# Optimization experiments

Hardware: AMD Instinct MI355X
Metric: run time of the kernel (lower is better)

## Reference

```python
import jax, jax.numpy as jnp
import numpy as np

WS = 4           # window_size
NUM_HEADS = 4
LN_EPS = 1e-5


def setup_inputs() -> dict:
    key = jax.random.key(0)
    ks = jax.random.split(key, 8)
    d = 256
    s = 0.02
    return {
        "feature": jax.random.normal(ks[0], (8, d, 127, 127), dtype=jnp.float32),
        "ln_w": jnp.ones((d,), jnp.float32),
        "ln_b": jnp.zeros((d,), jnp.float32),
        "in_w": jax.random.normal(ks[1], (3 * d, d), jnp.float32) * s,
        "in_b": jnp.zeros((3 * d,), jnp.float32),
        "out_w": jax.random.normal(ks[2], (d, d), jnp.float32) * s,
        "out_b": jnp.zeros((d,), jnp.float32),
        "proj_w": jax.random.normal(ks[3], (d, d), jnp.float32) * s,
        "proj_b": jnp.zeros((d,), jnp.float32),
    }


def reference(feature, ln_w, ln_b, in_w, in_b, out_w, out_b, proj_w, proj_b):
    B, C, H, W = feature.shape
    ws = WS
    pad_h = (-H) % ws
    pad_w = (-W) % ws
    x = jnp.pad(feature, ((0, 0), (0, 0), (0, pad_h), (0, pad_w)))
    Hp, Wp = H + pad_h, W + pad_w
    nh, nw = Hp // ws, Wp // ws
    # NCHW -> NHWC -> windows [B*nh*nw, ws*ws, C]
    x = x.transpose(0, 2, 3, 1)
    win = (x.reshape(B, nh, ws, nw, ws, C)
            .transpose(0, 1, 3, 2, 4, 5)
            .reshape(-1, ws * ws, C))
    # LayerNorm (ddof=0, matches torch)
    mu = win.mean(-1, keepdims=True)
    var = win.var(-1, keepdims=True)
    xn = (win - mu) / jnp.sqrt(var + LN_EPS) * ln_w + ln_b
    # fused QKV projection, then split heads
    qkv = xn @ in_w.T + in_b
    q, k, v = jnp.split(qkv, 3, axis=-1)
    hd = C // NUM_HEADS
    def heads(t):
        return t.reshape(t.shape[0], t.shape[1], NUM_HEADS, hd).transpose(0, 2, 1, 3)
    q, k, v = heads(q), heads(k), heads(v)
    scores = jnp.einsum('bhqd,bhkd->bhqk', q, k) / np.float32(np.sqrt(hd))
    a = jax.nn.softmax(scores, axis=-1)
    o = jnp.einsum('bhqk,bhkd->bhqd', a, v)
    o = o.transpose(0, 2, 1, 3).reshape(-1, ws * ws, C)
    o = o @ out_w.T + out_b
    # residual + Linear + exact GELU
    y = win + jax.nn.gelu(o @ proj_w.T + proj_b, approximate=False)
    # windows -> NHWC, crop padding, -> NCHW
    y = (y.reshape(B, nh, nw, ws, ws, C)
          .transpose(0, 1, 3, 2, 4, 5)
          .reshape(B, Hp, Wp, C))
    return y[:, :H, :W, :].transpose(0, 3, 1, 2)
```

## Files before the change

### kernel.cpp

```cpp
#include <hip/hip_runtime.h>

typedef _Float16 f16;
typedef __attribute__((ext_vector_type(4))) _Float16 half4;
typedef __attribute__((ext_vector_type(8))) _Float16 half8;
typedef __attribute__((ext_vector_type(4))) float f32x4;
typedef unsigned short u16;

#define MFMA32(a,b,c) __builtin_amdgcn_mfma_f32_16x16x32_f16(a,b,c,0,0,0)
#define MFMA16(a,b,c) __builtin_amdgcn_mfma_f32_16x16x16f16(a,b,c,0,0,0)

#define W_IN0   0
#define W_OUT0  196608
#define W_PROJ0 262144
#define X0      327680
#define QK0     33882112ull
#define VT0     100990976ull

__device__ __forceinline__ float gelu_f(float x) {
    float z = x * 0.70710678118f;
    float az = fabsf(z);
    float t = 1.f / (1.f + 0.3275911f * az);
    float e = __expf(-z * z);
    float poly = ((((1.061405429f * t - 1.453152027f) * t + 1.421413741f) * t
                   - 0.284496736f) * t + 0.254829592f) * t;
    float er = 1.f - poly * e;
    er = copysignf(er, z);
    return 0.5f * x * (1.f + er);
}

__global__ void k0_cast(const float* __restrict__ iw, const float* __restrict__ ow,
                        const float* __restrict__ pw, f16* __restrict__ W) {
    int i = blockIdx.x * 256 + threadIdx.x;
    if (i < 196608) W[W_IN0 + i] = (f16)iw[i];
    if (i < 16384) {
        const int s = i & 8191;
        const float* src = (i < 8192) ? ow : pw;
        f16* dst = W + ((i < 8192) ? W_OUT0 : W_PROJ0);
        const int g  = s & 3;
        const int r  = (s >> 2) & 31;
        const int kc = (s >> 7) & 7;
        const int ch = s >> 10;
        const int R = ch * 32 + r;
        const int c0 = kc * 32 + g * 4;
        f32x4 v0 = *(const f32x4*)(src + R * 256 + c0);
        f32x4 v1 = *(const f32x4*)(src + R * 256 + c0 + 16);
        half8 o;
#pragma unroll
        for (int j = 0; j < 4; ++j) { o[j] = (f16)v0[j]; o[j + 4] = (f16)v1[j]; }
        const int sg = g ^ ((r >> 1) & 3);
        *(half8*)(dst + ch * 8192 + kc * 1024 + r * 32 + sg * 8) = o;
    }
}

__global__ __launch_bounds__(256, 2)
void k1_pack(const float* __restrict__ feat, const float* __restrict__ lnw,
             const float* __restrict__ lnb, f16* __restrict__ X) {
    __shared__ float redS[256], redQ[256];
    const int tid = threadIdx.x;
    const int w = tid & 127, cq = tid >> 7;
    const int bid = blockIdx.x;
    const int bb = bid >> 7, h = bid & 127;
    const int c0 = cq * 128;
    const bool ok = (h < 127) && (w < 127);
    const size_t bbase = (size_t)bb * (256 * 127 * 127);
    const float* p0 = feat + bbase + (size_t)c0 * 16129 + (size_t)h * 127 + w;

    half8 ov[16];
    float s = 0.f, s2 = 0.f;
    if (ok) {
#pragma unroll
        for (int i = 0; i < 16; ++i) {
            half8 hv;
#pragma unroll
            for (int j = 0; j < 8; ++j) {
                float v = p0[(size_t)(i * 8 + j) * 16129];
                s += v; s2 += v * v; hv[j] = (f16)v;
            }
            ov[i] = hv;
        }
    } else {
#pragma unroll
        for (int i = 0; i < 16; ++i) {
            half8 hv;
#pragma unroll
            for (int j = 0; j < 8; ++j) hv[j] = (f16)0.f;
            ov[i] = hv;
        }
    }
    redS[tid] = s; redQ[tid] = s2;
    __syncthreads();
    float st = redS[w] + redS[w + 128];
    float qt = redQ[w] + redQ[w + 128];
    float mu = st * (1.f / 256.f);
    float rs = rsqrtf(qt * (1.f / 256.f) - mu * mu + 1e-5f);

    const int wi = h >> 2, hh = h & 3;
    const int jh = w >> 5, wl4 = (w >> 2) & 7, e = w & 3;
    const size_t t = ((size_t)((bb * 32 + wi) * 4 + jh)) * 128 + wl4 * 16 + hh * 4 + e;
    f16* xrow = X + t * 256 + c0;
#pragma unroll
    for (int i = 0; i < 16; ++i) {
        f32x4 lw0 = *(const f32x4*)(lnw + c0 + i * 8);
        f32x4 lw1 = *(const f32x4*)(lnw + c0 + i * 8 + 4);
        f32x4 lb0 = *(const f32x4*)(lnb + c0 + i * 8);
        f32x4 lb1 = *(const f32x4*)(lnb + c0 + i * 8 + 4);
        half8 o;
#pragma unroll
        for (int j = 0; j < 4; ++j) {
            o[j]     = (f16)(((float)ov[i][j]     - mu) * rs * lw0[j] + lb0[j]);
            o[j + 4] = (f16)(((float)ov[i][j + 4] - mu) * rs * lw1[j] + lb1[j]);
        }
        *(half8*)(xrow + i * 8) = o;
    }
}

__global__ __launch_bounds__(512, 2)
void k2_qkv(const f16* __restrict__ X, const f16* __restrict__ win,
            const float* __restrict__ inb, f16* __restrict__ QK, f16* __restrict__ VT) {
    __shared__ __align__(16) char sm[73728];
    const int tid = threadIdx.x, lane = tid & 63, wv = tid >> 6;
    const int nwg = gridDim.x;
    const int bid = (blockIdx.x & 7) * (nwg >> 3) + (blockIdx.x >> 3);
    const int mt = bid / 6, nb = bid % 6;
    const size_t Mbase = (size_t)mt * 256;
    const int n0 = nb * 128;
    const int wm = wv >> 1, wn = wv & 1;
    const int c = lane & 15, g = lane >> 4;
    const int chs = (lane & 3) ^ ((lane >> 3) & 3);

    f32x4 acc[4][4];
#pragma unroll
    for (int a = 0; a < 4; ++a)
#pragma unroll
        for (int b = 0; b < 4; ++b) acc[a][b] = f32x4{0.f, 0.f, 0.f, 0.f};

    auto stage = [&](int step, int bsel) {
        const f16* As = X + Mbase * 256 + step * 32;
        const f16* Bs = win + (size_t)n0 * 256 + step * 32;
        char* base = sm + bsel * 24576;
#pragma unroll
        for (int p = 0; p < 2; ++p) {
            int row = p * 128 + wv * 16 + (lane >> 2);
            __builtin_amdgcn_global_load_lds(
                (const __attribute__((address_space(1))) unsigned int*)(As + (size_t)row * 256 + chs * 8),
                (__attribute__((address_space(3))) unsigned int*)(base + p * 8192 + wv * 1024),
                16, 0, 0);
        }
        {
            int row = wv * 16 + (lane >> 2);
            __builtin_amdgcn_global_load_lds(
                (const __attribute__((address_space(1))) unsigned int*)(Bs + (size_t)row * 256 + chs * 8),
                (__attribute__((address_space(3))) unsigned int*)(base + 16384 + wv * 1024),
                16, 0, 0);
        }
    };
    const int rsl = (g ^ ((c >> 1) & 3)) * 16;
    auto compute = [&](int bsel) {
        char* base = sm + bsel * 24576;
        half8 a[4], b[4];
#pragma unroll
        for (int mi = 0; mi < 4; ++mi) {
            int row = wm * 64 + mi * 16 + c;
            a[mi] = *(half8*)(base + row * 64 + rsl);
        }
#pragma unroll
        for (int nt = 0; nt < 4; ++nt) {
            int row = wn * 64 + nt * 16 + c;
            b[nt] = *(half8*)(base + 16384 + row * 64 + rsl);
        }
#pragma unroll
        for (int mi = 0; mi < 4; ++mi)
#pragma unroll
            for (int nt = 0; nt < 4; ++nt)
                acc[mi][nt] = MFMA32(a[mi], b[nt], acc[mi][nt]);
    };

    stage(0, 0);
    stage(1, 1);
#pragma unroll
    for (int s = 0; s < 8; ++s) {
        if (s == 7) asm volatile("s_waitcnt vmcnt(0)" ::: "memory");
        else        asm volatile("s_waitcnt vmcnt(3)" ::: "memory");
        __builtin_amdgcn_s_barrier();
        if (s < 6) stage(s + 2, (s + 2) % 3);
        compute(s % 3);
    }

    const f32x4 z4 = {0.f, 0.f, 0.f, 0.f};
    half4 idf;
#pragma unroll
    for (int j = 0; j < 4; ++j) idf[j] = (f16)((g * 4 + j == c) ? 1.f : 0.f);

    if (n0 < 512) {
#pragma unroll
        for (int mi = 0; mi < 4; ++mi)
#pragma unroll
            for (int nt = 0; nt < 4; ++nt) {
                int n = n0 + wn * 64 + nt * 16 + c;
                float bias = inb[n];
                half4 h;
#pragma unroll
                for (int r = 0; r < 4; ++r) h[r] = (f16)(acc[mi][nt][r] + bias);
                f32x4 t = MFMA16(h, idf, z4);
                half4 o;
#pragma unroll
                for (int r = 0; r < 4; ++r) o[r] = (f16)t[r];
                size_t tok = Mbase + wm * 64 + mi * 16 + c;
                *(half4*)(QK + tok * 512 + (n0 + wn * 64 + nt * 16 + g * 4)) = o;
            }
    } else {
#pragma unroll
        for (int mi = 0; mi < 4; ++mi)
#pragma unroll
            for (int nt = 0; nt < 4; ++nt) {
                int n = n0 + wn * 64 + nt * 16 + c;
                float bias = inb[n];
                half4 h;
#pragma unroll
                for (int r = 0; r < 4; ++r) h[r] = (f16)(acc[mi][nt][r] + bias);
                int d = n - 512;
                size_t tokb = Mbase + wm * 64 + mi * 16;
                size_t winI = tokb >> 4;
                *(half4*)(VT + winI * 4096 + (size_t)d * 16 + g * 4) = h;
            }
    }
}

__global__ __launch_bounds__(256, 2)
void k3_attn(const f16* __restrict__ QK, const f16* __restrict__ VT,
             const f16* __restrict__ wout, const f16* __restrict__ wproj,
             const float* __restrict__ outb, const float* __restrict__ projb,
             f16* __restrict__ G) {
    __shared__ __align__(16) char sm[32768];
    const int tid = threadIdx.x, lane = tid & 63, wv = tid >> 6;
    const int c = lane & 15, g = lane >> 4;
    const size_t winA = (size_t)blockIdx.x * 8 + wv * 2;
    const size_t winB = winA + 1;
    const f16* qrowA = QK + (winA * 16 + c) * 512;
    const f16* qrowB = QK + (winB * 16 + c) * 512;
    const f32x4 z4 = {0.f, 0.f, 0.f, 0.f};

    auto stageW = [&](const f16* img, int rc, int bsel) {
#pragma unroll
        for (int q2 = 0; q2 < 4; ++q2) {
            int ia = wv * 4 + q2;
            __builtin_amdgcn_global_load_lds(
                (const __attribute__((address_space(1))) unsigned int*)(img + rc * 8192 + ia * 512 + lane * 8),
                (__attribute__((address_space(3))) unsigned int*)(sm + bsel * 16384 + ia * 1024),
                16, 0, 0);
        }
    };

    stageW(wout, 0, 0);

    half8 ofpA[4][2], ofpB[4][2];
#pragma unroll
    for (int wsel = 0; wsel < 2; ++wsel) {
        const f16* qrow = wsel ? qrowB : qrowA;
        const size_t wn_ = wsel ? winB : winA;
#pragma unroll
        for (int hq = 0; hq < 4; ++hq) {
            half8 af0 = *(const half8*)(qrow + 256 + hq * 64 + g * 8);
            half8 af1 = *(const half8*)(qrow + 256 + hq * 64 + 32 + g * 8);
            half8 bq0 = *(const half8*)(qrow + hq * 64 + g * 8);
            half8 bq1 = *(const half8*)(qrow + hq * 64 + 32 + g * 8);
            f32x4 sacc = MFMA32(af0, bq0, z4);
            sacc = MFMA32(af1, bq1, sacc);
            float s0 = sacc[0] * 0.125f, s1 = sacc[1] * 0.125f;
            float s2 = sacc[2] * 0.125f, s3 = sacc[3] * 0.125f;
            float mx = fmaxf(fmaxf(s0, s1), fmaxf(s2, s3));
            mx = fmaxf(mx, __shfl_xor(mx, 16));
            mx = fmaxf(mx, __shfl_xor(mx, 32));
            float p0 = __expf(s0 - mx), p1 = __expf(s1 - mx);
            float p2 = __expf(s2 - mx), p3 = __expf(s3 - mx);
            float sum = p0 + p1 + p2 + p3;
            sum += __shfl_xor(sum, 16);
            sum += __shfl_xor(sum, 32);
            float inv = 1.f / sum;
            half4 pf;
            pf[0] = (f16)(p0 * inv); pf[1] = (f16)(p1 * inv);
            pf[2] = (f16)(p2 * inv); pf[3] = (f16)(p3 * inv);
#pragma unroll
            for (int nt = 0; nt < 4; ++nt) {
                half4 vf = *(const half4*)(VT + wn_ * 4096 + (size_t)(hq * 64 + nt * 16 + c) * 16 + g * 4);
                f32x4 o = MFMA16(vf, pf, z4);
#pragma unroll
                for (int r = 0; r < 4; ++r) {
                    if (wsel) ofpB[hq][nt >> 1][(nt & 1) * 4 + r] = (f16)o[r];
                    else      ofpA[hq][nt >> 1][(nt & 1) * 4 + r] = (f16)o[r];
                }
            }
        }
    }

    const int rsl = (g ^ ((c >> 1) & 3)) * 16;
    half8 obpA[8], obpB[8];
    __syncthreads();

#pragma unroll
    for (int ch = 0; ch < 8; ++ch) {
        if (ch < 7) stageW(wout, ch + 1, (ch + 1) & 1);
        else        stageW(wproj, 0, (ch + 1) & 1);
        char* base = sm + (ch & 1) * 16384;
        f32x4 aA0 = z4, aA1 = z4, aB0 = z4, aB1 = z4;
#pragma unroll
        for (int kc = 0; kc < 8; ++kc) {
            half8 w0 = *(half8*)(base + kc * 2048 + c * 64 + rsl);
            aA0 = MFMA32(w0, ofpA[kc >> 1][kc & 1], aA0);
            aB0 = MFMA32(w0, ofpB[kc >> 1][kc & 1], aB0);
            half8 w1 = *(half8*)(base + kc * 2048 + 1024 + c * 64 + rsl);
            aA1 = MFMA32(w1, ofpA[kc >> 1][kc & 1], aA1);
            aB1 = MFMA32(w1, ofpB[kc >> 1][kc & 1], aB1);
        }
        f32x4 b0 = *(const f32x4*)(outb + ch * 32 + g * 4);
        f32x4 b1 = *(const f32x4*)(outb + ch * 32 + 16 + g * 4);
#pragma unroll
        for (int r = 0; r < 4; ++r) {
            obpA[ch][r]     = (f16)(aA0[r] + b0[r]);
            obpA[ch][4 + r] = (f16)(aA1[r] + b1[r]);
            obpB[ch][r]     = (f16)(aB0[r] + b0[r]);
            obpB[ch][4 + r] = (f16)(aB1[r] + b1[r]);
        }
        __syncthreads();
    }

#pragma unroll
    for (int pc = 0; pc < 8; ++pc) {
        if (pc < 7) stageW(wproj, pc + 1, (pc + 1) & 1);
        char* base = sm + (pc & 1) * 16384;
        f32x4 aA0 = z4, aA1 = z4, aB0 = z4, aB1 = z4;
#pragma unroll
        for (int kc = 0; kc < 8; ++kc) {
            half8 w0 = *(half8*)(base + kc * 2048 + c * 64 + rsl);
            aA0 = MFMA32(w0, obpA[kc], aA0);
            aB0 = MFMA32(w0, obpB[kc], aB0);
            half8 w1 = *(half8*)(base + kc * 2048 + 1024 + c * 64 + rsl);
            aA1 = MFMA32(w1, obpA[kc], aA1);
            aB1 = MFMA32(w1, obpB[kc], aB1);
        }
        f32x4 b0 = *(const f32x4*)(projb + pc * 32 + g * 4);
        f32x4 b1 = *(const f32x4*)(projb + pc * 32 + 16 + g * 4);
        half4 hA0, hA1, hB0, hB1;
#pragma unroll
        for (int r = 0; r < 4; ++r) {
            hA0[r] = (f16)gelu_f(aA0[r] + b0[r]);
            hA1[r] = (f16)gelu_f(aA1[r] + b1[r]);
            hB0[r] = (f16)gelu_f(aB0[r] + b0[r]);
            hB1[r] = (f16)gelu_f(aB1[r] + b1[r]);
        }
        f16* growA = G + (winA * 16 + c) * 256 + pc * 32;
        *(half4*)(growA + g * 4) = hA0;
        *(half4*)(growA + 16 + g * 4) = hA1;
        f16* growB = G + (winB * 16 + c) * 256 + pc * 32;
        *(half4*)(growB + g * 4) = hB0;
        *(half4*)(growB + 16 + g * 4) = hB1;
        if (pc < 7) __syncthreads();
    }
}

__global__ __launch_bounds__(256, 8)
void k4_out(const f16* __restrict__ G, const float* __restrict__ feat, float* __restrict__ outp) {
    const int tid = threadIdx.x;
    const int bid = blockIdx.x;
    const int bb = bid / 127, h = bid % 127;
    const int w = tid & 127;
    const int cq = tid >> 7;
    const bool wok = (w < 127);
    const size_t bbase = (size_t)bb * (256 * 127 * 127);
    const int wi = h >> 2, hh = h & 3;
    const int jh = w >> 5, wl4 = (w >> 2) & 7, e = w & 3;
    const size_t t = ((size_t)((bb * 32 + wi) * 4 + jh)) * 128 + wl4 * 16 + hh * 4 + e;
    const f16* gp = G + t * 256;
    const float* fp = feat + bbase + (size_t)h * 127 + w;
    float* op = outp + bbase + (size_t)h * 127 + w;
#pragma unroll 4
    for (int ci = 0; ci < 32; ++ci) {
        const int ch = ci * 8 + cq * 4;
        if (wok) {
            half4 g4 = *(const half4*)(gp + ch);
#pragma unroll
            for (int j = 0; j < 4; ++j) {
                size_t off = (size_t)(ch + j) * 16129;
                op[off] = fp[off] + (float)g4[j];
            }
        }
    }
}

extern "C" void kernel_launch(void* const* d_in, const int* in_sizes, int n_in,
                              void* d_out, int out_size, void* d_ws, size_t ws_size,
                              hipStream_t stream) {
    const float* feat   = (const float*)d_in[0];
    const float* ln_w   = (const float*)d_in[1];
    const float* ln_b   = (const float*)d_in[2];
    const float* in_w   = (const float*)d_in[3];
    const float* in_b   = (const float*)d_in[4];
    const float* out_w  = (const float*)d_in[5];
    const float* out_b  = (const float*)d_in[6];
    const float* proj_w = (const float*)d_in[7];
    const float* proj_b = (const float*)d_in[8];

    f16* W  = (f16*)d_ws;
    f16* Xb  = W + X0;
    f16* QKb = W + QK0;
    f16* VTb = W + VT0;
    f16* Gb  = Xb;

    k0_cast<<<768, 256, 0, stream>>>(in_w, out_w, proj_w, W);
    k1_pack<<<1024, 256, 0, stream>>>(feat, ln_w, ln_b, Xb);
    k2_qkv<<<3072, 512, 0, stream>>>(Xb, W + W_IN0, in_b, QKb, VTb);
    k3_attn<<<1024, 256, 0, stream>>>(QKb, VTb, W + W_OUT0, W + W_PROJ0, out_b, proj_b, Gb);
    k4_out<<<1016, 256, 0, stream>>>(Gb, feat, (float*)d_out);
}
```

Baseline: 336.9 us.

## Triple-buffer weight staging in attention kernel and raise MFMA priority

The attention kernel's out-proj and proj weight streaming becomes a single 16-step loop with a triple-buffered LDS ring. It uses explicit vmcnt waits and one barrier per step instead of double buffering with two __syncthreads per chunk. s_setprio is raised around the MFMA blocks in both the QKV GEMM and the attention kernel so matrix work gets issue priority over other waves. LDS use grows from 32KB to 48KB per block, which may limit occupancy. The hand-counted vmcnt values must match the in-flight global stores and loads.

```diff
diff --git a/kernel.cpp b/kernel.cpp
--- a/kernel.cpp
+++ b/kernel.cpp
@@ -168,11 +168,13 @@
             int row = wn * 64 + nt * 16 + c;
             b[nt] = *(half8*)(base + 16384 + row * 64 + rsl);
         }
+        __builtin_amdgcn_s_setprio(1);
 #pragma unroll
         for (int mi = 0; mi < 4; ++mi)
 #pragma unroll
             for (int nt = 0; nt < 4; ++nt)
                 acc[mi][nt] = MFMA32(a[mi], b[nt], acc[mi][nt]);
+        __builtin_amdgcn_s_setprio(0);
     };
 
     stage(0, 0);
@@ -231,7 +233,7 @@
              const f16* __restrict__ wout, const f16* __restrict__ wproj,
              const float* __restrict__ outb, const float* __restrict__ projb,
              f16* __restrict__ G) {
-    __shared__ __align__(16) char sm[32768];
+    __shared__ __align__(16) char sm[49152];
     const int tid = threadIdx.x, lane = tid & 63, wv = tid >> 6;
     const int c = lane & 15, g = lane >> 4;
     const size_t winA = (size_t)blockIdx.x * 8 + wv * 2;
@@ -240,18 +242,20 @@
     const f16* qrowB = QK + (winB * 16 + c) * 512;
     const f32x4 z4 = {0.f, 0.f, 0.f, 0.f};
 
-    auto stageW = [&](const f16* img, int rc, int bsel) {
+    auto stageW = [&](int it, int bsel) {
+        const f16* img = (it < 8) ? (wout + it * 8192) : (wproj + (it - 8) * 8192);
 #pragma unroll
         for (int q2 = 0; q2 < 4; ++q2) {
             int ia = wv * 4 + q2;
             __builtin_amdgcn_global_load_lds(
-                (const __attribute__((address_space(1))) unsigned int*)(img + rc * 8192 + ia * 512 + lane * 8),
+                (const __attribute__((address_space(1))) unsigned int*)(img + ia * 512 + lane * 8),
                 (__attribute__((address_space(3))) unsigned int*)(sm + bsel * 16384 + ia * 1024),
                 16, 0, 0);
         }
     };
 
-    stageW(wout, 0, 0);
+    stageW(0, 0);
+    stageW(1, 1);
 
     half8 ofpA[4][2], ofpB[4][2];
 #pragma unroll
@@ -295,66 +299,69 @@
 
     const int rsl = (g ^ ((c >> 1) & 3)) * 16;
     half8 obpA[8], obpB[8];
-    __syncthreads();
-
-#pragma unroll
-    for (int ch = 0; ch < 8; ++ch) {
-        if (ch < 7) stageW(wout, ch + 1, (ch + 1) & 1);
-        else        stageW(wproj, 0, (ch + 1) & 1);
-        char* base = sm + (ch & 1) * 16384;
+
+#pragma unroll
+    for (int it = 0; it < 16; ++it) {
+        if (it == 15)     asm volatile("s_waitcnt vmcnt(4)" ::: "memory");
+        else if (it >= 9) asm volatile("s_waitcnt vmcnt(8)" ::: "memory");
+        else              asm volatile("s_waitcnt vmcnt(4)" ::: "memory");
+        __builtin_amdgcn_s_barrier();
+        if (it < 14) stageW(it + 2, (it + 2) % 3);
+        char* base = sm + (it % 3) * 16384;
         f32x4 aA0 = z4, aA1 = z4, aB0 = z4, aB1 = z4;
-#pragma unroll
-        for (int kc = 0; kc < 8; ++kc) {
-            half8 w0 = *(half8*)(base + kc * 2048 + c * 64 + rsl);
-            aA0 = MFMA32(w0, ofpA[kc >> 1][kc & 1], aA0);
-            aB0 = MFMA32(w0, ofpB[kc >> 1][kc & 1], aB0);
-            half8 w1 = *(half8*)(base + kc * 2048 + 1024 + c * 64 + rsl);
-            aA1 = MFMA32(w1, ofpA[kc >> 1][kc & 1], aA1);
-            aB1 = MFMA32(w1, ofpB[kc >> 1][kc & 1], aB1);
-        }
-        f32x4 b0 = *(const f32x4*)(outb + ch * 32 + g * 4);
-        f32x4 b1 = *(const f32x4*)(outb + ch * 32 + 16 + g * 4);
-#pragma unroll
-        for (int r = 0; r < 4; ++r) {
-            obpA[ch][r]     = (f16)(aA0[r] + b0[r]);
-            obpA[ch][4 + r] = (f16)(aA1[r] + b1[r]);
-            obpB[ch][r]     = (f16)(aB0[r] + b0[r]);
-            obpB[ch][4 + r] = (f16)(aB1[r] + b1[r]);
-        }
-        __syncthreads();
-    }
-
-#pragma unroll
-    for (int pc = 0; pc < 8; ++pc) {
-        if (pc < 7) stageW(wproj, pc + 1, (pc + 1) & 1);
-        char* base = sm + (pc & 1) * 16384;
-        f32x4 aA0 = z4, aA1 = z4, aB0 = z4, aB1 = z4;
-#pragma unroll
-        for (int kc = 0; kc < 8; ++kc) {
-            half8 w0 = *(half8*)(base + kc * 2048 + c * 64 + rsl);
-            aA0 = MFMA32(w0, obpA[kc], aA0);
-            aB0 = MFMA32(w0, obpB[kc], aB0);
-            half8 w1 = *(half8*)(base + kc * 2048 + 1024 + c * 64 + rsl);
-            aA1 = MFMA32(w1, obpA[kc], aA1);
-            aB1 = MFMA32(w1, obpB[kc], aB1);
-        }
-        f32x4 b0 = *(const f32x4*)(projb + pc * 32 + g * 4);
-        f32x4 b1 = *(const f32x4*)(projb + pc * 32 + 16 + g * 4);
-        half4 hA0, hA1, hB0, hB1;
-#pragma unroll
-        for (int r = 0; r < 4; ++r) {
-            hA0[r] = (f16)gelu_f(aA0[r] + b0[r]);
-            hA1[r] = (f16)gelu_f(aA1[r] + b1[r]);
-            hB0[r] = (f16)gelu_f(aB0[r] + b0[r]);
-            hB1[r] = (f16)gelu_f(aB1[r] + b1[r]);
-        }
-        f16* growA = G + (winA * 16 + c) * 256 + pc * 32;
-        *(half4*)(growA + g * 4) = hA0;
-        *(half4*)(growA + 16 + g * 4) = hA1;
-        f16* growB = G + (winB * 16 + c) * 256 + pc * 32;
-        *(half4*)(growB + g * 4) = hB0;
-        *(half4*)(growB + 16 + g * 4) = hB1;
-        if (pc < 7) __syncthreads();
+        __builtin_amdgcn_s_setprio(1);
+        if (it < 8) {
+#pragma unroll
+            for (int kc = 0; kc < 8; ++kc) {
+                half8 w0 = *(half8*)(base + kc * 2048 + c * 64 + rsl);
+                aA0 = MFMA32(w0, ofpA[kc >> 1][kc & 1], aA0);
+                aB0 = MFMA32(w0, ofpB[kc >> 1][kc & 1], aB0);
+                half8 w1 = *(half8*)(base + kc * 2048 + 1024 + c * 64 + rsl);
+                aA1 = MFMA32(w1, ofpA[kc >> 1][kc & 1], aA1);
+                aB1 = MFMA32(w1, ofpB[kc >> 1][kc & 1], aB1);
+            }
+        } else {
+#pragma unroll
+            for (int kc = 0; kc < 8; ++kc) {
+                half8 w0 = *(half8*)(base + kc * 2048 + c * 64 + rsl);
+                aA0 = MFMA32(w0, obpA[kc], aA0);
+                aB0 = MFMA32(w0, obpB[kc], aB0);
+                half8 w1 = *(half8*)(base + kc * 2048 + 1024 + c * 64 + rsl);
+                aA1 = MFMA32(w1, obpA[kc], aA1);
+                aB1 = MFMA32(w1, obpB[kc], aB1);
+            }
+        }
+        __builtin_amdgcn_s_setprio(0);
+        if (it < 8) {
+            const int ch = it;
+            f32x4 b0 = *(const f32x4*)(outb + ch * 32 + g * 4);
+            f32x4 b1 = *(const f32x4*)(outb + ch * 32 + 16 + g * 4);
+#pragma unroll
+            for (int r = 0; r < 4; ++r) {
+                obpA[ch][r]     = (f16)(aA0[r] + b0[r]);
+                obpA[ch][4 + r] = (f16)(aA1[r] + b1[r]);
+                obpB[ch][r]     = (f16)(aB0[r] + b0[r]);
+                obpB[ch][4 + r] = (f16)(aB1[r] + b1[r]);
+            }
+        } else {
+            const int pc = it - 8;
+            f32x4 b0 = *(const f32x4*)(projb + pc * 32 + g * 4);
+            f32x4 b1 = *(const f32x4*)(projb + pc * 32 + 16 + g * 4);
+            half4 hA0, hA1, hB0, hB1;
+#pragma unroll
+            for (int r = 0; r < 4; ++r) {
+                hA0[r] = (f16)gelu_f(aA0[r] + b0[r]);
+                hA1[r] = (f16)gelu_f(aA1[r] + b1[r]);
+                hB0[r] = (f16)gelu_f(aB0[r] + b0[r]);
+                hB1[r] = (f16)gelu_f(aB1[r] + b1[r]);
+            }
+            f16* growA = G + (winA * 16 + c) * 256 + pc * 32;
+            *(half4*)(growA + g * 4) = hA0;
+            *(half4*)(growA + 16 + g * 4) = hA1;
+            f16* growB = G + (winB * 16 + c) * 256 + pc * 32;
+            *(half4*)(growB + g * 4) = hB0;
+            *(half4*)(growB + 16 + g * 4) = hB1;
+        }
     }
 }
 
```

Result: no change. 333.4 us (-1.0%).
